# Performance work log

Measured on AMD Instinct MI355X. Metric: run time of the kernel, lower is better.

## Reference

```python
import jax, jax.numpy as jnp
import numpy as np

OUTPUT_DIM = 2000
INPUT_DIM = 8192
N_COLS = 2000  # must equal OUTPUT_DIM so bias broadcasts over last dim as in the torch code
SPARSITY = 0.9
BLOCK = 4


def _apply_block_sparsity(weight, block=BLOCK, sparsity=SPARSITY, seed=1234):
    # Zero out 4x4 blocks with probability `sparsity`, mirroring apply_block_sparsity.
    rng = np.random.RandomState(seed)
    rb = (weight.shape[0] + block - 1) // block
    cb = (weight.shape[1] + block - 1) // block
    keep = (rng.rand(rb, cb) <= (1.0 - sparsity)).astype(np.float32)
    mask = np.kron(keep, np.ones((block, block), dtype=np.float32))
    return weight * mask[: weight.shape[0], : weight.shape[1]]


def setup_inputs() -> dict:
    key = jax.random.key(0)
    k_w, k_b, k_x = jax.random.split(key, 3)
    weight = np.asarray(jax.random.normal(k_w, (OUTPUT_DIM, INPUT_DIM), dtype=jnp.float32))
    weight = jnp.asarray(_apply_block_sparsity(weight))
    bias = jax.random.normal(k_b, (OUTPUT_DIM,), dtype=jnp.float32)
    x = jax.random.normal(k_x, (INPUT_DIM, N_COLS), dtype=jnp.float32)
    return {"weight": weight, "bias": bias, "x": x}


def reference(weight, bias, x):
    # [OUT, IN] @ [IN, N] -> [OUT, N]; bias [OUT] broadcasts over last dim (N == OUT here),
    # exactly matching torch.matmul(weight, x) + bias.
    return jnp.matmul(weight, x) + bias
```

## Files before the change

kernel.cpp:

```cpp
#include <hip/hip_runtime.h>

#define K_DIM 8192
#define M_REAL 2000
#define N_REAL 2000
#define M_PAD 2048
#define N_PAD 2048

#define BM 128
#define BN 128
#define BK 32
#define SPLITK 4
#define KSLAB (K_DIM / SPLITK)
#define NSTEP (KSLAB / BK)

#define NB_W 1024
#define NB_X 2048
#define NB_I 256

typedef __bf16 bf16x8 __attribute__((ext_vector_type(8)));
typedef float f32x4 __attribute__((ext_vector_type(4)));
typedef float fvec4 __attribute__((ext_vector_type(4)));

__device__ __forceinline__ unsigned short f2bf(float f) {
    union { float f; unsigned u; } v; v.f = f;
    unsigned r = v.u + 0x7FFFu + ((v.u >> 16) & 1u);
    return (unsigned short)(r >> 16);
}

__device__ __forceinline__ unsigned pk2(float a, float b) {
    return (unsigned)f2bf(a) | ((unsigned)f2bf(b) << 16);
}

__device__ __forceinline__ void async16(const void* g, void* l) {
    __builtin_amdgcn_global_load_lds((__attribute__((address_space(1))) void*)(g),
                                     (__attribute__((address_space(3))) void*)(l),
                                     16, 0, 0);
}

__global__ __launch_bounds__(256) void prep_kernel(const float* __restrict__ W,
                                                   const float* __restrict__ X,
                                                   const float* __restrict__ bias,
                                                   unsigned short* __restrict__ Wb,
                                                   unsigned short* __restrict__ XT,
                                                   float* __restrict__ out) {
    __shared__ unsigned short T[64][130];
    int bid = blockIdx.x;
    if (bid < NB_W) {
        unsigned tid = bid * 256u + threadIdx.x;
#pragma unroll
        for (unsigned i = 0; i < 8; ++i) {
            unsigned e = (i * (1024u * 256u) + tid) * 8u;
            uint4 o = make_uint4(0u, 0u, 0u, 0u);
            if (e < (unsigned)(M_REAL * K_DIM)) {
                fvec4 f0 = __builtin_nontemporal_load((const fvec4*)(W + e));
                fvec4 f1 = __builtin_nontemporal_load((const fvec4*)(W + e + 4));
                o.x = pk2(f0.x, f0.y);
                o.y = pk2(f0.z, f0.w);
                o.z = pk2(f1.x, f1.y);
                o.w = pk2(f1.z, f1.w);
            }
            *(uint4*)(Wb + e) = o;
        }
    } else if (bid < NB_W + NB_X) {
        int b = bid - NB_W;
        int k0 = (b & 63) << 7;
        int n0 = (b >> 6) << 6;
        int t = threadIdx.x;
        int c = t & 15;
        int r = t >> 4;
        int nl = c << 2;
        int n = n0 + nl;
        bool valid = (n < N_REAL);
#pragma unroll
        for (int p = 0; p < 4; ++p) {
            int kl = (r << 1) + (p << 5);
            fvec4 v0 = {0.f, 0.f, 0.f, 0.f};
            fvec4 v1 = {0.f, 0.f, 0.f, 0.f};
            if (valid) {
                v0 = __builtin_nontemporal_load((const fvec4*)(X + (k0 + kl) * N_REAL + n));
                v1 = __builtin_nontemporal_load((const fvec4*)(X + (k0 + kl + 1) * N_REAL + n));
            }
            *(unsigned*)&T[nl + 0][kl] = pk2(v0.x, v1.x);
            *(unsigned*)&T[nl + 1][kl] = pk2(v0.y, v1.y);
            *(unsigned*)&T[nl + 2][kl] = pk2(v0.z, v1.z);
            *(unsigned*)&T[nl + 3][kl] = pk2(v0.w, v1.w);
        }
        __syncthreads();
#pragma unroll
        for (int it = 0; it < 4; ++it) {
            int nl2 = r + (it << 4);
            int kl2 = c << 3;
            const unsigned* tp = (const unsigned*)&T[nl2][kl2];
            uint4 o;
            o.x = tp[0]; o.y = tp[1]; o.z = tp[2]; o.w = tp[3];
            *(uint4*)(XT + (((n0 + nl2) << 13) + k0 + kl2)) = o;
        }
    } else {
        const int total = M_REAL * (N_REAL / 4);
        for (int i = (bid - NB_W - NB_X) * 256 + (int)threadIdx.x; i < total; i += NB_I * 256) {
            int m = i / (N_REAL / 4);
            int n4 = i - m * (N_REAL / 4);
            float4 bv = *(const float4*)(bias + (n4 << 2));
            *(float4*)(out + m * N_REAL + (n4 << 2)) = bv;
        }
    }
}

__global__ __launch_bounds__(256, 4) void gemm_kernel(const unsigned short* __restrict__ Wb,
                                                      const unsigned short* __restrict__ XT,
                                                      float* __restrict__ out) {
    __shared__ __align__(16) char smA[2 * 8192];
    __shared__ __align__(16) char smB[2 * 8192];

    int f = blockIdx.x;
    int xcd = f & 7;
    int local = f >> 3;
    int bz = local & 3;
    int lt = local >> 2;
    int bx = (xcd & 3) * 4 + (lt & 3);
    int by = (xcd >> 2) * 8 + (lt >> 2);

    int t = threadIdx.x;
    int w = t >> 6;
    int l = t & 63;
    int lane16 = l & 15;
    int quad = l >> 4;
    int wr = w >> 1;
    int wc = w & 1;
    int m0 = by * BM;
    int n0 = bx * BN;
    int ks = bz * KSLAB;

    f32x4 acc[4][4] = {};

    int rowS = w * 32 + (l >> 2);
    int lc   = (l & 3) ^ ((l >> 3) & 3);
    const unsigned short* gA0 = Wb + (long long)(m0 + rowS) * K_DIM + ks + lc * 8;
    const unsigned short* gA1 = gA0 + 16LL * K_DIM;
    const unsigned short* gB0 = XT + (long long)(n0 + rowS) * K_DIM + ks + lc * 8;
    const unsigned short* gB1 = gB0 + 16LL * K_DIM;

#define STAGE(BUF, KOFF) do { \
        int bo_ = (BUF) * 8192 + w * 2048; \
        async16(gA0 + (KOFF), smA + bo_); \
        async16(gA1 + (KOFF), smA + bo_ + 1024); \
        async16(gB0 + (KOFF), smB + bo_); \
        async16(gB1 + (KOFF), smB + bo_ + 1024); \
    } while (0)

    int swz = ((quad ^ ((lane16 >> 1) & 3)) << 4);
    int arow = (wr * 64 + lane16) * 64 + swz;
    int brow = (wc * 64 + lane16) * 64 + swz;

    STAGE(0, 0);
    __syncthreads();

    for (int s = 0; s < NSTEP; ++s) {
        if (s + 1 < NSTEP)
            STAGE((s + 1) & 1, (s + 1) * BK);

        int bo = (s & 1) * 8192;
        const char* Ab = smA + bo + arow;
        const char* Bb = smB + bo + brow;
        bf16x8 a0 = *(const bf16x8*)(Ab);
        bf16x8 a1 = *(const bf16x8*)(Ab + 1024);
        bf16x8 a2 = *(const bf16x8*)(Ab + 2048);
        bf16x8 a3 = *(const bf16x8*)(Ab + 3072);
        bf16x8 b0 = *(const bf16x8*)(Bb);
        bf16x8 b1 = *(const bf16x8*)(Bb + 1024);
        bf16x8 b2 = *(const bf16x8*)(Bb + 2048);
        bf16x8 b3 = *(const bf16x8*)(Bb + 3072);

        acc[0][0] = __builtin_amdgcn_mfma_f32_16x16x32_bf16(a0, b0, acc[0][0], 0, 0, 0);
        acc[0][1] = __builtin_amdgcn_mfma_f32_16x16x32_bf16(a0, b1, acc[0][1], 0, 0, 0);
        acc[0][2] = __builtin_amdgcn_mfma_f32_16x16x32_bf16(a0, b2, acc[0][2], 0, 0, 0);
        acc[0][3] = __builtin_amdgcn_mfma_f32_16x16x32_bf16(a0, b3, acc[0][3], 0, 0, 0);
        acc[1][0] = __builtin_amdgcn_mfma_f32_16x16x32_bf16(a1, b0, acc[1][0], 0, 0, 0);
        acc[1][1] = __builtin_amdgcn_mfma_f32_16x16x32_bf16(a1, b1, acc[1][1], 0, 0, 0);
        acc[1][2] = __builtin_amdgcn_mfma_f32_16x16x32_bf16(a1, b2, acc[1][2], 0, 0, 0);
        acc[1][3] = __builtin_amdgcn_mfma_f32_16x16x32_bf16(a1, b3, acc[1][3], 0, 0, 0);
        acc[2][0] = __builtin_amdgcn_mfma_f32_16x16x32_bf16(a2, b0, acc[2][0], 0, 0, 0);
        acc[2][1] = __builtin_amdgcn_mfma_f32_16x16x32_bf16(a2, b1, acc[2][1], 0, 0, 0);
        acc[2][2] = __builtin_amdgcn_mfma_f32_16x16x32_bf16(a2, b2, acc[2][2], 0, 0, 0);
        acc[2][3] = __builtin_amdgcn_mfma_f32_16x16x32_bf16(a2, b3, acc[2][3], 0, 0, 0);
        acc[3][0] = __builtin_amdgcn_mfma_f32_16x16x32_bf16(a3, b0, acc[3][0], 0, 0, 0);
        acc[3][1] = __builtin_amdgcn_mfma_f32_16x16x32_bf16(a3, b1, acc[3][1], 0, 0, 0);
        acc[3][2] = __builtin_amdgcn_mfma_f32_16x16x32_bf16(a3, b2, acc[3][2], 0, 0, 0);
        acc[3][3] = __builtin_amdgcn_mfma_f32_16x16x32_bf16(a3, b3, acc[3][3], 0, 0, 0);

        if (s + 1 < NSTEP)
            __syncthreads();
    }
#undef STAGE

#pragma unroll
    for (int j = 0; j < 4; ++j) {
        int n = n0 + wc * 64 + j * 16 + lane16;
        if (n >= N_REAL) continue;
#pragma unroll
        for (int i = 0; i < 4; ++i) {
            int mbase = m0 + wr * 64 + i * 16 + quad * 4;
#pragma unroll
            for (int r = 0; r < 4; ++r) {
                int m = mbase + r;
                if (m < M_REAL)
                    atomicAdd(&out[(long long)m * N_REAL + n], acc[i][j][r]);
            }
        }
    }
}

extern "C" void kernel_launch(void* const* d_in, const int* in_sizes, int n_in,
                              void* d_out, int out_size, void* d_ws, size_t ws_size,
                              hipStream_t stream) {
    const float* W    = (const float*)d_in[0];
    const float* bias = (const float*)d_in[1];
    const float* X    = (const float*)d_in[2];
    float* out = (float*)d_out;

    unsigned short* Wb = (unsigned short*)d_ws;
    unsigned short* XT = Wb + (long long)M_PAD * K_DIM;

    prep_kernel<<<NB_W + NB_X + NB_I, 256, 0, stream>>>(W, X, bias, Wb, XT, out);

    gemm_kernel<<<(N_PAD / BN) * (M_PAD / BM) * SPLITK, 256, 0, stream>>>(Wb, XT, out);
}
```

Before: 259.0 us.

## Drop split-K in favour of 512-thread blocks with direct bias-fused stores

Removes the 4-way split-K and its fp32 atomicAdd epilogue. Each 128x128 tile is now computed by one 512-thread block of 8 waves (2x4 wave grid, 64x32 per wave), which adds bias and writes output with plain stores. The bias pre-fill pass in the prep kernel is dropped. The trade-off is only 256 blocks across the device and a four-times-longer K loop per block, against the removal of atomic traffic and the output pre-initialisation pass.

```diff
diff --git a/kernel.cpp b/kernel.cpp
--- a/kernel.cpp
+++ b/kernel.cpp
@@ -9,13 +9,10 @@
 #define BM 128
 #define BN 128
 #define BK 32
-#define SPLITK 4
-#define KSLAB (K_DIM / SPLITK)
-#define NSTEP (KSLAB / BK)
+#define NSTEP (K_DIM / BK)
 
 #define NB_W 1024
 #define NB_X 2048
-#define NB_I 256
 
 typedef __bf16 bf16x8 __attribute__((ext_vector_type(8)));
 typedef float f32x4 __attribute__((ext_vector_type(4)));
@@ -39,10 +36,8 @@
 
 __global__ __launch_bounds__(256) void prep_kernel(const float* __restrict__ W,
                                                    const float* __restrict__ X,
-                                                   const float* __restrict__ bias,
                                                    unsigned short* __restrict__ Wb,
-                                                   unsigned short* __restrict__ XT,
-                                                   float* __restrict__ out) {
+                                                   unsigned short* __restrict__ XT) {
     __shared__ unsigned short T[64][130];
     int bid = blockIdx.x;
     if (bid < NB_W) {
@@ -61,7 +56,7 @@
             }
             *(uint4*)(Wb + e) = o;
         }
-    } else if (bid < NB_W + NB_X) {
+    } else {
         int b = bid - NB_W;
         int k0 = (b & 63) << 7;
         int n0 = (b >> 6) << 6;
@@ -95,19 +90,12 @@
             o.x = tp[0]; o.y = tp[1]; o.z = tp[2]; o.w = tp[3];
             *(uint4*)(XT + (((n0 + nl2) << 13) + k0 + kl2)) = o;
         }
-    } else {
-        const int total = M_REAL * (N_REAL / 4);
-        for (int i = (bid - NB_W - NB_X) * 256 + (int)threadIdx.x; i < total; i += NB_I * 256) {
-            int m = i / (N_REAL / 4);
-            int n4 = i - m * (N_REAL / 4);
-            float4 bv = *(const float4*)(bias + (n4 << 2));
-            *(float4*)(out + m * N_REAL + (n4 << 2)) = bv;
-        }
     }
 }
 
-__global__ __launch_bounds__(256, 4) void gemm_kernel(const unsigned short* __restrict__ Wb,
+__global__ __launch_bounds__(512, 2) void gemm_kernel(const unsigned short* __restrict__ Wb,
                                                       const unsigned short* __restrict__ XT,
+                                                      const float* __restrict__ bias,
                                                       float* __restrict__ out) {
     __shared__ __align__(16) char smA[2 * 8192];
     __shared__ __align__(16) char smB[2 * 8192];
@@ -115,42 +103,35 @@
     int f = blockIdx.x;
     int xcd = f & 7;
     int local = f >> 3;
-    int bz = local & 3;
-    int lt = local >> 2;
-    int bx = (xcd & 3) * 4 + (lt & 3);
-    int by = (xcd >> 2) * 8 + (lt >> 2);
+    int bx = (xcd & 3) * 4 + (local & 3);
+    int by = (xcd >> 2) * 8 + (local >> 2);
 
     int t = threadIdx.x;
     int w = t >> 6;
     int l = t & 63;
     int lane16 = l & 15;
     int quad = l >> 4;
-    int wr = w >> 1;
-    int wc = w & 1;
+    int wr = w >> 2;
+    int wc = w & 3;
     int m0 = by * BM;
     int n0 = bx * BN;
-    int ks = bz * KSLAB;
 
-    f32x4 acc[4][4] = {};
+    f32x4 acc[4][2] = {};
 
-    int rowS = w * 32 + (l >> 2);
-    int lc   = (l & 3) ^ ((l >> 3) & 3);
-    const unsigned short* gA0 = Wb + (long long)(m0 + rowS) * K_DIM + ks + lc * 8;
-    const unsigned short* gA1 = gA0 + 16LL * K_DIM;
-    const unsigned short* gB0 = XT + (long long)(n0 + rowS) * K_DIM + ks + lc * 8;
-    const unsigned short* gB1 = gB0 + 16LL * K_DIM;
+    int rowS = t >> 2;
+    int lc   = (t & 3) ^ ((t >> 3) & 3);
+    const unsigned short* gA = Wb + (long long)(m0 + rowS) * K_DIM + lc * 8;
+    const unsigned short* gB = XT + (long long)(n0 + rowS) * K_DIM + lc * 8;
 
 #define STAGE(BUF, KOFF) do { \
-        int bo_ = (BUF) * 8192 + w * 2048; \
-        async16(gA0 + (KOFF), smA + bo_); \
-        async16(gA1 + (KOFF), smA + bo_ + 1024); \
-        async16(gB0 + (KOFF), smB + bo_); \
-        async16(gB1 + (KOFF), smB + bo_ + 1024); \
+        int bo_ = (BUF) * 8192 + w * 1024; \
+        async16(gA + (KOFF), smA + bo_); \
+        async16(gB + (KOFF), smB + bo_); \
     } while (0)
 
     int swz = ((quad ^ ((lane16 >> 1) & 3)) << 4);
     int arow = (wr * 64 + lane16) * 64 + swz;
-    int brow = (wc * 64 + lane16) * 64 + swz;
+    int brow = (wc * 32 + lane16) * 64 + swz;
 
     STAGE(0, 0);
     __syncthreads();
@@ -168,25 +149,15 @@
         bf16x8 a3 = *(const bf16x8*)(Ab + 3072);
         bf16x8 b0 = *(const bf16x8*)(Bb);
         bf16x8 b1 = *(const bf16x8*)(Bb + 1024);
-        bf16x8 b2 = *(const bf16x8*)(Bb + 2048);
-        bf16x8 b3 = *(const bf16x8*)(Bb + 3072);
 
         acc[0][0] = __builtin_amdgcn_mfma_f32_16x16x32_bf16(a0, b0, acc[0][0], 0, 0, 0);
         acc[0][1] = __builtin_amdgcn_mfma_f32_16x16x32_bf16(a0, b1, acc[0][1], 0, 0, 0);
-        acc[0][2] = __builtin_amdgcn_mfma_f32_16x16x32_bf16(a0, b2, acc[0][2], 0, 0, 0);
-        acc[0][3] = __builtin_amdgcn_mfma_f32_16x16x32_bf16(a0, b3, acc[0][3], 0, 0, 0);
         acc[1][0] = __builtin_amdgcn_mfma_f32_16x16x32_bf16(a1, b0, acc[1][0], 0, 0, 0);
         acc[1][1] = __builtin_amdgcn_mfma_f32_16x16x32_bf16(a1, b1, acc[1][1], 0, 0, 0);
-        acc[1][2] = __builtin_amdgcn_mfma_f32_16x16x32_bf16(a1, b2, acc[1][2], 0, 0, 0);
-        acc[1][3] = __builtin_amdgcn_mfma_f32_16x16x32_bf16(a1, b3, acc[1][3], 0, 0, 0);
         acc[2][0] = __builtin_amdgcn_mfma_f32_16x16x32_bf16(a2, b0, acc[2][0], 0, 0, 0);
         acc[2][1] = __builtin_amdgcn_mfma_f32_16x16x32_bf16(a2, b1, acc[2][1], 0, 0, 0);
-        acc[2][2] = __builtin_amdgcn_mfma_f32_16x16x32_bf16(a2, b2, acc[2][2], 0, 0, 0);
-        acc[2][3] = __builtin_amdgcn_mfma_f32_16x16x32_bf16(a2, b3, acc[2][3], 0, 0, 0);
         acc[3][0] = __builtin_amdgcn_mfma_f32_16x16x32_bf16(a3, b0, acc[3][0], 0, 0, 0);
         acc[3][1] = __builtin_amdgcn_mfma_f32_16x16x32_bf16(a3, b1, acc[3][1], 0, 0, 0);
-        acc[3][2] = __builtin_amdgcn_mfma_f32_16x16x32_bf16(a3, b2, acc[3][2], 0, 0, 0);
-        acc[3][3] = __builtin_amdgcn_mfma_f32_16x16x32_bf16(a3, b3, acc[3][3], 0, 0, 0);
 
         if (s + 1 < NSTEP)
             __syncthreads();
@@ -194,9 +165,10 @@
 #undef STAGE
 
 #pragma unroll
-    for (int j = 0; j < 4; ++j) {
-        int n = n0 + wc * 64 + j * 16 + lane16;
+    for (int j = 0; j < 2; ++j) {
+        int n = n0 + wc * 32 + j * 16 + lane16;
         if (n >= N_REAL) continue;
+        float bv = bias[n];
 #pragma unroll
         for (int i = 0; i < 4; ++i) {
             int mbase = m0 + wr * 64 + i * 16 + quad * 4;
@@ -204,7 +176,7 @@
             for (int r = 0; r < 4; ++r) {
                 int m = mbase + r;
                 if (m < M_REAL)
-                    atomicAdd(&out[(long long)m * N_REAL + n], acc[i][j][r]);
+                    out[(long long)m * N_REAL + n] = acc[i][j][r] + bv;
             }
         }
     }
@@ -221,7 +193,7 @@
     unsigned short* Wb = (unsigned short*)d_ws;
     unsigned short* XT = Wb + (long long)M_PAD * K_DIM;
 
-    prep_kernel<<<NB_W + NB_X + NB_I, 256, 0, stream>>>(W, X, bias, Wb, XT, out);
+    prep_kernel<<<NB_W + NB_X, 256, 0, stream>>>(W, X, Wb, XT);
 
-    gemm_kernel<<<(N_PAD / BN) * (M_PAD / BM) * SPLITK, 256, 0, stream>>>(Wb, XT, out);
+    gemm_kernel<<<(N_PAD / BN) * (M_PAD / BM), 512, 0, stream>>>(Wb, XT, bias, out);
 }
```

Result: slower. 274.2 us (+5.8%).

## Fuse W bf16 conversion into GEMM A-load, use split-K=2 with separate reduce

Applied to the files above, without the earlier changes.

The separate pass that converts W to bf16 is removed. The GEMM now loads fp32 W rows directly into registers two steps ahead, converts them to bf16 and writes them swizzled into shared memory, while X still goes through the async LDS path. Split-K drops from 4 to 2, and the atomicAdd epilogue is replaced by plain stores of partials plus a reduce kernel that adds the two partials and the bias. This removes a bf16 W round-trip through memory and the atomic contention, at the cost of more register pressure, synchronous A loads in the main loop, and a third kernel launch.

```diff
diff --git a/kernel.cpp b/kernel.cpp
--- a/kernel.cpp
+++ b/kernel.cpp
@@ -9,13 +9,9 @@
 #define BM 128
 #define BN 128
 #define BK 32
-#define SPLITK 4
+#define SPLITK 2
 #define KSLAB (K_DIM / SPLITK)
 #define NSTEP (KSLAB / BK)
-
-#define NB_W 1024
-#define NB_X 2048
-#define NB_I 256
 
 typedef __bf16 bf16x8 __attribute__((ext_vector_type(8)));
 typedef float f32x4 __attribute__((ext_vector_type(4)));
@@ -37,86 +33,55 @@
                                      16, 0, 0);
 }
 
-__global__ __launch_bounds__(256) void prep_kernel(const float* __restrict__ W,
-                                                   const float* __restrict__ X,
-                                                   const float* __restrict__ bias,
-                                                   unsigned short* __restrict__ Wb,
-                                                   unsigned short* __restrict__ XT,
-                                                   float* __restrict__ out) {
+__global__ __launch_bounds__(256) void prep_x(const float* __restrict__ X,
+                                              unsigned short* __restrict__ XT) {
     __shared__ unsigned short T[64][130];
-    int bid = blockIdx.x;
-    if (bid < NB_W) {
-        unsigned tid = bid * 256u + threadIdx.x;
-#pragma unroll
-        for (unsigned i = 0; i < 8; ++i) {
-            unsigned e = (i * (1024u * 256u) + tid) * 8u;
-            uint4 o = make_uint4(0u, 0u, 0u, 0u);
-            if (e < (unsigned)(M_REAL * K_DIM)) {
-                fvec4 f0 = __builtin_nontemporal_load((const fvec4*)(W + e));
-                fvec4 f1 = __builtin_nontemporal_load((const fvec4*)(W + e + 4));
-                o.x = pk2(f0.x, f0.y);
-                o.y = pk2(f0.z, f0.w);
-                o.z = pk2(f1.x, f1.y);
-                o.w = pk2(f1.z, f1.w);
-            }
-            *(uint4*)(Wb + e) = o;
+    int b = blockIdx.x;
+    int k0 = (b & 63) << 7;
+    int n0 = (b >> 6) << 6;
+    int t = threadIdx.x;
+    int c = t & 15;
+    int r = t >> 4;
+    int nl = c << 2;
+    int n = n0 + nl;
+    bool valid = (n < N_REAL);
+#pragma unroll
+    for (int p = 0; p < 4; ++p) {
+        int kl = (r << 1) + (p << 5);
+        fvec4 v0 = {0.f, 0.f, 0.f, 0.f};
+        fvec4 v1 = {0.f, 0.f, 0.f, 0.f};
+        if (valid) {
+            v0 = __builtin_nontemporal_load((const fvec4*)(X + (k0 + kl) * N_REAL + n));
+            v1 = __builtin_nontemporal_load((const fvec4*)(X + (k0 + kl + 1) * N_REAL + n));
         }
-    } else if (bid < NB_W + NB_X) {
-        int b = bid - NB_W;
-        int k0 = (b & 63) << 7;
-        int n0 = (b >> 6) << 6;
-        int t = threadIdx.x;
-        int c = t & 15;
-        int r = t >> 4;
-        int nl = c << 2;
-        int n = n0 + nl;
-        bool valid = (n < N_REAL);
-#pragma unroll
-        for (int p = 0; p < 4; ++p) {
-            int kl = (r << 1) + (p << 5);
-            fvec4 v0 = {0.f, 0.f, 0.f, 0.f};
-            fvec4 v1 = {0.f, 0.f, 0.f, 0.f};
-            if (valid) {
-                v0 = __builtin_nontemporal_load((const fvec4*)(X + (k0 + kl) * N_REAL + n));
-                v1 = __builtin_nontemporal_load((const fvec4*)(X + (k0 + kl + 1) * N_REAL + n));
-            }
-            *(unsigned*)&T[nl + 0][kl] = pk2(v0.x, v1.x);
-            *(unsigned*)&T[nl + 1][kl] = pk2(v0.y, v1.y);
-            *(unsigned*)&T[nl + 2][kl] = pk2(v0.z, v1.z);
-            *(unsigned*)&T[nl + 3][kl] = pk2(v0.w, v1.w);
-        }
-        __syncthreads();
-#pragma unroll
-        for (int it = 0; it < 4; ++it) {
-            int nl2 = r + (it << 4);
-            int kl2 = c << 3;
-            const unsigned* tp = (const unsigned*)&T[nl2][kl2];
-            uint4 o;
-            o.x = tp[0]; o.y = tp[1]; o.z = tp[2]; o.w = tp[3];
-            *(uint4*)(XT + (((n0 + nl2) << 13) + k0 + kl2)) = o;
-        }
-    } else {
-        const int total = M_REAL * (N_REAL / 4);
-        for (int i = (bid - NB_W - NB_X) * 256 + (int)threadIdx.x; i < total; i += NB_I * 256) {
-            int m = i / (N_REAL / 4);
-            int n4 = i - m * (N_REAL / 4);
-            float4 bv = *(const float4*)(bias + (n4 << 2));
-            *(float4*)(out + m * N_REAL + (n4 << 2)) = bv;
-        }
-    }
-}
-
-__global__ __launch_bounds__(256, 4) void gemm_kernel(const unsigned short* __restrict__ Wb,
+        *(unsigned*)&T[nl + 0][kl] = pk2(v0.x, v1.x);
+        *(unsigned*)&T[nl + 1][kl] = pk2(v0.y, v1.y);
+        *(unsigned*)&T[nl + 2][kl] = pk2(v0.z, v1.z);
+        *(unsigned*)&T[nl + 3][kl] = pk2(v0.w, v1.w);
+    }
+    __syncthreads();
+#pragma unroll
+    for (int it = 0; it < 4; ++it) {
+        int nl2 = r + (it << 4);
+        int kl2 = c << 3;
+        const unsigned* tp = (const unsigned*)&T[nl2][kl2];
+        uint4 o;
+        o.x = tp[0]; o.y = tp[1]; o.z = tp[2]; o.w = tp[3];
+        *(uint4*)(XT + (((n0 + nl2) << 13) + k0 + kl2)) = o;
+    }
+}
+
+__global__ __launch_bounds__(256, 4) void gemm_kernel(const float* __restrict__ W,
                                                       const unsigned short* __restrict__ XT,
-                                                      float* __restrict__ out) {
+                                                      float* __restrict__ part) {
     __shared__ __align__(16) char smA[2 * 8192];
     __shared__ __align__(16) char smB[2 * 8192];
 
     int f = blockIdx.x;
     int xcd = f & 7;
     int local = f >> 3;
-    int bz = local & 3;
-    int lt = local >> 2;
+    int bz = local & 1;
+    int lt = local >> 1;
     int bx = (xcd & 3) * 4 + (lt & 3);
     int by = (xcd >> 2) * 8 + (lt >> 2);
 
@@ -132,18 +97,46 @@
     int ks = bz * KSLAB;
 
     f32x4 acc[4][4] = {};
+    const fvec4 z4 = {0.f, 0.f, 0.f, 0.f};
+
+    int rA = t >> 1;
+    int hA = t & 1;
+    int rowA = m0 + rA;
+    bool aValid = (rowA < M_REAL);
+    const float* gW = W + (long long)(aValid ? rowA : 0) * K_DIM + ks + hA * 16;
+    int swA = (rA >> 1) & 3;
+    int dA0 = rA * 64 + (((hA << 1) | 0) ^ swA) * 16;
+    int dA1 = rA * 64 + (((hA << 1) | 1) ^ swA) * 16;
+
+    fvec4 wreg0, wreg1, wreg2, wreg3;
+
+#define LOADA(S) do { \
+        const float* p_ = gW + (S) * BK; \
+        wreg0 = *(const fvec4*)(p_); \
+        wreg1 = *(const fvec4*)(p_ + 4); \
+        wreg2 = *(const fvec4*)(p_ + 8); \
+        wreg3 = *(const fvec4*)(p_ + 12); \
+        if (!aValid) { wreg0 = z4; wreg1 = z4; wreg2 = z4; wreg3 = z4; } \
+    } while (0)
+
+#define WRITEA(BUF) do { \
+        int bo_ = (BUF) * 8192; \
+        uint4 u0, u1; \
+        u0.x = pk2(wreg0.x, wreg0.y); u0.y = pk2(wreg0.z, wreg0.w); \
+        u0.z = pk2(wreg1.x, wreg1.y); u0.w = pk2(wreg1.z, wreg1.w); \
+        u1.x = pk2(wreg2.x, wreg2.y); u1.y = pk2(wreg2.z, wreg2.w); \
+        u1.z = pk2(wreg3.x, wreg3.y); u1.w = pk2(wreg3.z, wreg3.w); \
+        *(uint4*)(smA + bo_ + dA0) = u0; \
+        *(uint4*)(smA + bo_ + dA1) = u1; \
+    } while (0)
 
     int rowS = w * 32 + (l >> 2);
     int lc   = (l & 3) ^ ((l >> 3) & 3);
-    const unsigned short* gA0 = Wb + (long long)(m0 + rowS) * K_DIM + ks + lc * 8;
-    const unsigned short* gA1 = gA0 + 16LL * K_DIM;
     const unsigned short* gB0 = XT + (long long)(n0 + rowS) * K_DIM + ks + lc * 8;
     const unsigned short* gB1 = gB0 + 16LL * K_DIM;
 
-#define STAGE(BUF, KOFF) do { \
+#define STAGEB(BUF, KOFF) do { \
         int bo_ = (BUF) * 8192 + w * 2048; \
-        async16(gA0 + (KOFF), smA + bo_); \
-        async16(gA1 + (KOFF), smA + bo_ + 1024); \
         async16(gB0 + (KOFF), smB + bo_); \
         async16(gB1 + (KOFF), smB + bo_ + 1024); \
     } while (0)
@@ -152,12 +145,19 @@
     int arow = (wr * 64 + lane16) * 64 + swz;
     int brow = (wc * 64 + lane16) * 64 + swz;
 
-    STAGE(0, 0);
+    LOADA(0);
+    WRITEA(0);
+    LOADA(1);
+    STAGEB(0, 0);
     __syncthreads();
 
     for (int s = 0; s < NSTEP; ++s) {
-        if (s + 1 < NSTEP)
-            STAGE((s + 1) & 1, (s + 1) * BK);
+        if (s + 1 < NSTEP) {
+            STAGEB((s + 1) & 1, (s + 1) * BK);
+            WRITEA((s + 1) & 1);
+        }
+        if (s + 2 < NSTEP)
+            LOADA(s + 2);
 
         int bo = (s & 1) * 8192;
         const char* Ab = smA + bo + arow;
@@ -191,22 +191,35 @@
         if (s + 1 < NSTEP)
             __syncthreads();
     }
-#undef STAGE
-
+#undef LOADA
+#undef WRITEA
+#undef STAGEB
+
+    float* pb = part + ((long long)bz << 22);
 #pragma unroll
     for (int j = 0; j < 4; ++j) {
         int n = n0 + wc * 64 + j * 16 + lane16;
-        if (n >= N_REAL) continue;
 #pragma unroll
         for (int i = 0; i < 4; ++i) {
             int mbase = m0 + wr * 64 + i * 16 + quad * 4;
 #pragma unroll
-            for (int r = 0; r < 4; ++r) {
-                int m = mbase + r;
-                if (m < M_REAL)
-                    atomicAdd(&out[(long long)m * N_REAL + n], acc[i][j][r]);
-            }
+            for (int r = 0; r < 4; ++r)
+                pb[(long long)(mbase + r) * 2048 + n] = acc[i][j][r];
         }
+    }
+}
+
+__global__ __launch_bounds__(256) void reduce_kernel(const float* __restrict__ part,
+                                                     const float* __restrict__ bias,
+                                                     float* __restrict__ out) {
+    int m = blockIdx.x;
+    const float* p0 = part + (long long)m * 2048;
+    for (int n4 = threadIdx.x; n4 < N_REAL / 4; n4 += 256) {
+        fvec4 s0 = *(const fvec4*)(p0 + n4 * 4);
+        fvec4 s1 = *(const fvec4*)(p0 + 4194304 + n4 * 4);
+        fvec4 bv = *(const fvec4*)(bias + n4 * 4);
+        fvec4 r = s0 + s1 + bv;
+        *(fvec4*)(out + (long long)m * N_REAL + n4 * 4) = r;
     }
 }
 
@@ -218,10 +231,10 @@
     const float* X    = (const float*)d_in[2];
     float* out = (float*)d_out;
 
-    unsigned short* Wb = (unsigned short*)d_ws;
-    unsigned short* XT = Wb + (long long)M_PAD * K_DIM;
-
-    prep_kernel<<<NB_W + NB_X + NB_I, 256, 0, stream>>>(W, X, bias, Wb, XT, out);
-
-    gemm_kernel<<<(N_PAD / BN) * (M_PAD / BM) * SPLITK, 256, 0, stream>>>(Wb, XT, out);
-}
+    unsigned short* XT = (unsigned short*)d_ws;
+    float* part = (float*)((char*)d_ws + (size_t)M_PAD * K_DIM * 2);
+
+    prep_x<<<2048, 256, 0, stream>>>(X, XT);
+    gemm_kernel<<<(N_PAD / BN) * (M_PAD / BM) * SPLITK, 256, 0, stream>>>(W, XT, part);
+    reduce_kernel<<<M_REAL, 256, 0, stream>>>(part, bias, out);
+}
```

Result: slower. 323.0 us (+24.7%).
